# Kernel tuning notes

Measured on AMD Instinct MI355X. Metric: run time of the kernel, lower is better.

The kernel has to match this reference:

```python
import jax, jax.numpy as jnp
import numpy as np

N_ITER = 8192
N_CHANNELS = 64

def setup_inputs() -> dict:
    key = jax.random.key(0)
    x = jax.random.normal(key, (128, N_ITER * N_CHANNELS), dtype=jnp.float32)
    s_init = jnp.zeros((N_CHANNELS,), dtype=jnp.float32)
    return {"x": x, "s_init": s_init}

def reference(x, s_init):
    # CumSumLoop: slice last dim into n_iter blocks of n_channels,
    # running sum carried across blocks, initialized with s_init.
    B = x.shape[0]
    xb = x.reshape(B, N_ITER, N_CHANNELS)          # [B, n_iter, C]
    y = jnp.cumsum(xb, axis=1) + s_init            # s_init added to every prefix (first step: x_0 + s_init)
    return y.reshape(B, N_ITER * N_CHANNELS)
```

## Files before the change

### kernel.cpp

```cpp
#include <hip/hip_runtime.h>


typedef float f4 __attribute__((ext_vector_type(4)));

#define B    128
#define T    8192
#define C    64
#define NC   64
#define L    (T / NC)
#define ROW4 (C / 4)
#define CH4  (L * ROW4)

__global__ __launch_bounds__(256) void k_partial(const f4* __restrict__ x,
                                                 f4* __restrict__ out) {
    const int tid   = blockIdx.x * 256 + threadIdx.x;
    const int chunk = tid >> 4;
    const int g     = tid & 15;
    const size_t base = (size_t)chunk * CH4 + g;
    f4 s = {0.f, 0.f, 0.f, 0.f};
    #pragma unroll 8
    for (int t = 0; t < L; ++t)
        s += x[base + (size_t)t * ROW4];
    out[base] = s;
}

__global__ __launch_bounds__(256) void k_scan(const f4* __restrict__ s_init,
                                              f4* __restrict__ out) {
    const int tid = blockIdx.x * 256 + threadIdx.x;
    const int b   = tid >> 4;
    const int g   = tid & 15;
    f4 off = s_init[g];
    size_t idx = (size_t)b * NC * CH4 + g;
    #pragma unroll 4
    for (int k = 0; k < NC; ++k, idx += CH4) {
        const f4 p = out[idx];
        out[idx] = off;
        off += p;
    }
}

__global__ __launch_bounds__(256) void k_write(const f4* __restrict__ x,
                                               f4* __restrict__ out) {
    const int tid   = blockIdx.x * 256 + threadIdx.x;
    const int chunk = tid >> 4;
    const int g     = tid & 15;
    const size_t base = (size_t)chunk * CH4 + g;
    f4 run = out[base];
    #pragma unroll 8
    for (int t = 0; t < L; ++t) {
        run += x[base + (size_t)t * ROW4];
        __builtin_nontemporal_store(run, &out[base + (size_t)t * ROW4]);
    }
}

extern "C" void kernel_launch(void* const* d_in, const int* in_sizes, int n_in,
                              void* d_out, int out_size, void* d_ws, size_t ws_size,
                              hipStream_t stream) {
    const f4* x      = (const f4*)d_in[0];
    const f4* s_init = (const f4*)d_in[1];
    f4* out          = (f4*)d_out;

    dim3 blk(256);
    dim3 grd1((B * NC * 16) / 256);
    dim3 grd2((B * 16) / 256);

    k_partial<<<grd1, blk, 0, stream>>>(x, out);
    k_scan   <<<grd2, blk, 0, stream>>>(s_init, out);
    k_write  <<<grd1, blk, 0, stream>>>(x, out);
}
```

Baseline: 479.5 us.

## Replace three-pass scan with single-pass chained scan using dynamic tickets

Adds a single-pass decoupled-lookback style kernel. Each block takes a ticket, loads its chunk into registers, computes a block-local scan in shared memory, and publishes its chunk aggregate with a release flag. It then waits on the flags of earlier chunks for the same batch row and sums their aggregates to get its offset. This removes the second full read of x and the partial-sum round trip through global memory, at the cost of spin-waiting, a timeout fallback that recomputes from x, and a dependence on workspace being large enough. The original three-kernel path is kept as a fallback when the workspace is too small.

```diff
diff --git a/kernel.cpp b/kernel.cpp
--- a/kernel.cpp
+++ b/kernel.cpp
@@ -3,13 +3,124 @@
 
 typedef float f4 __attribute__((ext_vector_type(4)));
 
-#define B    128
-#define T    8192
-#define C    64
-#define NC   64
-#define L    (T / NC)
-#define ROW4 (C / 4)
-#define CH4  (L * ROW4)
+#define B      128
+#define T      8192
+#define NC     64
+#define L      (T / NC)
+#define ROW4   16
+#define CH4    (L * ROW4)
+#define NCHUNK (B * NC)
+#define VPT    (L / 16)
+
+#define FLAGS_OFF_U32 64
+#define AGG_OFF_U32   8256
+#define WS_NEED       (33024u + (size_t)NCHUNK * 16 * sizeof(f4))
+
+__global__ __launch_bounds__(256) void k_init(uint32_t* __restrict__ ws) {
+    const int i = blockIdx.x * 256 + threadIdx.x;
+    if (i == 0) ws[0] = 0u;
+    if (i < NCHUNK) ws[FLAGS_OFF_U32 + i] = 0u;
+}
+
+__global__ __launch_bounds__(256) void k_onepass(const f4* __restrict__ x,
+                                                 const f4* __restrict__ s_init,
+                                                 f4* __restrict__ out,
+                                                 uint32_t* __restrict__ ws) {
+    __shared__ f4 tot[16][16];
+    __shared__ f4 off_lds[16];
+    __shared__ uint32_t tkt_lds;
+
+    uint32_t* counter = ws;
+    uint32_t* flags   = ws + FLAGS_OFF_U32;
+    f4*       agg     = (f4*)(ws + AGG_OFF_U32);
+
+    const int tid = threadIdx.x;
+    if (tid == 0) tkt_lds = atomicAdd(counter, 1u);
+    __syncthreads();
+    const uint32_t ticket = tkt_lds;
+    const int b   = (int)(ticket & (B - 1));
+    const int k   = (int)(ticket >> 7);
+    const int cid = b * NC + k;
+
+    const int s = tid >> 4;
+    const int g = tid & 15;
+
+    const size_t base = (size_t)cid * CH4 + (size_t)(s * VPT) * ROW4 + g;
+
+    f4 v[VPT];
+    #pragma unroll
+    for (int i = 0; i < VPT; ++i)
+        v[i] = __builtin_nontemporal_load(&x[base + (size_t)i * ROW4]);
+
+    f4 tsum = v[0];
+    #pragma unroll
+    for (int i = 1; i < VPT; ++i) tsum += v[i];
+
+    tot[s][g] = tsum;
+    __syncthreads();
+    f4 acc = tsum;
+    #pragma unroll
+    for (int d = 1; d < 16; d <<= 1) {
+        if (s >= d) acc += tot[s - d][g];
+        __syncthreads();
+        tot[s][g] = acc;
+        __syncthreads();
+    }
+
+    if (s == 15) {
+        agg[(size_t)cid * 16 + g] = acc;
+        __threadfence();
+        if (g == 0)
+            __hip_atomic_store(&flags[cid], 1u, __ATOMIC_RELEASE,
+                               __HIP_MEMORY_SCOPE_AGENT);
+    }
+
+    if (tid < 64) {
+        const int gg    = tid & 15;
+        const int kk_of = tid >> 4;
+        f4 a = {0.f, 0.f, 0.f, 0.f};
+        if (kk_of == 0) a = s_init[gg];
+        for (int kk0 = 0; kk0 < k; kk0 += 4) {
+            const int kk = kk0 + kk_of;
+            if (kk < k) {
+                const int pid = b * NC + kk;
+                uint32_t spins = 0;
+                bool ok = true;
+                while (__hip_atomic_load(&flags[pid], __ATOMIC_ACQUIRE,
+                                         __HIP_MEMORY_SCOPE_AGENT) == 0u) {
+                    __builtin_amdgcn_s_sleep(2);
+                    if (++spins > (1u << 20)) { ok = false; break; }
+                }
+                if (ok) {
+                    a += agg[(size_t)pid * 16 + gg];
+                } else {
+                    const size_t pb = (size_t)pid * CH4 + gg;
+                    f4 t = {0.f, 0.f, 0.f, 0.f};
+                    for (int tt = 0; tt < L; ++tt)
+                        t += x[pb + (size_t)tt * ROW4];
+                    a += t;
+                }
+            }
+        }
+        #pragma unroll
+        for (int m = 16; m <= 32; m <<= 1) {
+            a.x += __shfl_xor(a.x, m, 64);
+            a.y += __shfl_xor(a.y, m, 64);
+            a.z += __shfl_xor(a.z, m, 64);
+            a.w += __shfl_xor(a.w, m, 64);
+        }
+        if (tid < 16) off_lds[tid] = a;
+    }
+    __syncthreads();
+
+    f4 run = off_lds[g];
+    if (s > 0) run += tot[s - 1][g];
+    #pragma unroll
+    for (int i = 0; i < VPT; ++i) {
+        run += v[i];
+        __builtin_nontemporal_store(run, &out[base + (size_t)i * ROW4]);
+    }
+}
 
 __global__ __launch_bounds__(256) void k_partial(const f4* __restrict__ x,
                                                  f4* __restrict__ out) {
@@ -32,7 +143,7 @@
     f4 off = s_init[g];
     size_t idx = (size_t)b * NC * CH4 + g;
     #pragma unroll 4
-    for (int k = 0; k < NC; ++k, idx += CH4) {
+    for (int kk = 0; kk < NC; ++kk, idx += CH4) {
         const f4 p = out[idx];
         out[idx] = off;
         off += p;
@@ -60,11 +171,14 @@
     const f4* s_init = (const f4*)d_in[1];
     f4* out          = (f4*)d_out;
 
-    dim3 blk(256);
-    dim3 grd1((B * NC * 16) / 256);
-    dim3 grd2((B * 16) / 256);
-
-    k_partial<<<grd1, blk, 0, stream>>>(x, out);
-    k_scan   <<<grd2, blk, 0, stream>>>(s_init, out);
-    k_write  <<<grd1, blk, 0, stream>>>(x, out);
+    if (d_ws != nullptr && ws_size >= WS_NEED) {
+        uint32_t* ws = (uint32_t*)d_ws;
+        k_init   <<<dim3((NCHUNK + 255) / 256), dim3(256), 0, stream>>>(ws);
+        k_onepass<<<dim3(NCHUNK), dim3(256), 0, stream>>>(x, s_init, out, ws);
+    } else {
+        dim3 blk(256);
+        k_partial<<<dim3(512), blk, 0, stream>>>(x, out);
+        k_scan   <<<dim3(8),   blk, 0, stream>>>(s_init, out);
+        k_write  <<<dim3(512), blk, 0, stream>>>(x, out);
+    }
 }
```

After: 1.477 ms. +208.1%, slower.
